# Optimization experiments

Hardware: AMD Instinct MI355X
Metric: run time of the kernel (lower is better)

The kernel has to match this reference:

```python
import jax, jax.numpy as jnp
import numpy as np

B, T, H, W, DIN = 8, 16, 32, 32, 384
DOUT = 384
K = 2  # kernel_size == stride == downsample_ratio


def setup_inputs() -> dict:
    key = jax.random.key(0)
    ks = jax.random.split(key, 12)
    s_in = 1.0 / np.sqrt(DIN)
    s_out = 1.0 / np.sqrt(DOUT)
    s_hid = 1.0 / np.sqrt(2 * DOUT)
    return {
        "x": jax.random.normal(ks[0], (B, T, H, W, DIN), dtype=jnp.float32),
        "Wq": jax.random.normal(ks[1], (DIN, DOUT), dtype=jnp.float32) * s_in,
        "bq": jnp.zeros((DOUT,), jnp.float32),
        "Wk": jax.random.normal(ks[2], (DIN, DOUT), dtype=jnp.float32) * s_in,
        "bk": jnp.zeros((DOUT,), jnp.float32),
        "Wv": jax.random.normal(ks[3], (DIN, DOUT), dtype=jnp.float32) * s_in,
        "bv": jnp.zeros((DOUT,), jnp.float32),
        "W1": jax.random.normal(ks[4], (DOUT, 2 * DOUT), dtype=jnp.float32) * s_out,
        "b1": jnp.zeros((2 * DOUT,), jnp.float32),
        "W2": jax.random.normal(ks[5], (2 * DOUT, DOUT), dtype=jnp.float32) * s_hid,
        "b2": jnp.zeros((DOUT,), jnp.float32),
        "gamma": jnp.ones((DOUT,), jnp.float32),
        "beta": jnp.zeros((DOUT,), jnp.float32),
    }


def _forward(x, Wq, bq, Wk, bk, Wv, bv, W1, b1, W2, b2, gamma, beta):
    b, t, h, w, d = x.shape
    nh, nw = h // K, w // K
    # window partition: (b*t, nh*nw, K*K, d)
    xw = x.reshape(b * t, nh, K, nw, K, d).transpose(0, 1, 3, 2, 4, 5)
    xw = xw.reshape(b * t, nh * nw, K * K, d)
    # mean-query local attention
    q = xw.mean(axis=2, keepdims=True) @ Wq + bq          # (bt, N, 1, D)
    k = xw @ Wk + bk                                       # (bt, N, K*K, D)
    v = xw @ Wv + bv                                       # (bt, N, K*K, D)
    scale = DOUT ** (-0.5)
    attn = jnp.einsum('bnqd,bnkd->bnqk', q, k) * scale     # (bt, N, 1, K*K)
    attn = jax.nn.softmax(attn, axis=-1)
    out = jnp.einsum('bnqk,bnkd->bnqd', attn, v)[:, :, 0]  # (bt, N, D)
    out = out.reshape(b, t, nh, nw, DOUT)
    # refine: Linear-GELU-Linear-LayerNorm (exact erf GELU, eps=1e-5)
    hdn = jax.nn.gelu(out @ W1 + b1, approximate=False)
    y = hdn @ W2 + b2
    mu = y.mean(axis=-1, keepdims=True)
    var = y.var(axis=-1, keepdims=True)
    y = (y - mu) * jax.lax.rsqrt(var + 1e-5) * gamma + beta
    return y


def reference(x, Wq, bq, Wk, bk, Wv, bv, W1, b1, W2, b2, gamma, beta):
    return _forward(x, Wq, bq, Wk, bk, Wv, bv, W1, b1, W2, b2, gamma, beta)
```

## Files before the change

### kernel.cpp

```cpp
#include <hip/hip_runtime.h>
#include <hip/hip_bf16.h>
#include <math.h>

typedef unsigned short u16;
typedef __attribute__((ext_vector_type(8))) short short8;
typedef __attribute__((ext_vector_type(4))) float f32x4;
typedef __attribute__((ext_vector_type(4))) unsigned short u16x4;

#define NWIN 32768
#define ROWSTRIDE (32*384)

__device__ __forceinline__ float b2f(u16 v) {
  unsigned int u = ((unsigned int)v) << 16;
  return __builtin_bit_cast(float, u);
}
__device__ __forceinline__ u16 f2b(float f) {
  unsigned int u = __builtin_bit_cast(unsigned int, f);
  unsigned int r = (u + 0x7fffu + ((u >> 16) & 1u)) >> 16;
  return (u16)r;
}

__global__ void fold_qk(const float* __restrict__ Wq, const float* __restrict__ Wk,
                        u16* __restrict__ WqkT) {
  __shared__ float a[16][17];
  __shared__ float b[16][17];
  const int tx = threadIdx.x, ty = threadIdx.y;
  const int k0 = blockIdx.x * 16, n0 = blockIdx.y * 16;
  float acc = 0.f;
  for (int d0 = 0; d0 < 384; d0 += 16) {
    a[ty][tx] = Wk[(n0 + ty) * 384 + d0 + tx];
    b[ty][tx] = Wq[(k0 + ty) * 384 + d0 + tx];
    __syncthreads();
#pragma unroll
    for (int dd = 0; dd < 16; ++dd) acc += a[ty][dd] * b[tx][dd];
    __syncthreads();
  }
  WqkT[(n0 + ty) * 384 + k0 + tx] = f2b(acc);
}

__global__ void bias_qk(const float* __restrict__ bq, const float* __restrict__ Wk,
                        float* __restrict__ bqk) {
  const int n = blockIdx.x * 128 + threadIdx.x;
  float s = 0.f;
  for (int d = 0; d < 384; ++d) s += bq[d] * Wk[n * 384 + d];
  bqk[n] = s;
}

__global__ void fold_v1(const float* __restrict__ Wv, const float* __restrict__ W1,
                        u16* __restrict__ W1pT) {
  __shared__ float a[16][17];
  __shared__ float b[16][17];
  const int tx = threadIdx.x, ty = threadIdx.y;
  const int n0 = blockIdx.x * 16, k0 = blockIdx.y * 16;
  float acc = 0.f;
  for (int d0 = 0; d0 < 384; d0 += 16) {
    a[ty][tx] = W1[(d0 + ty) * 768 + n0 + tx];
    b[ty][tx] = Wv[(k0 + ty) * 384 + d0 + tx];
    __syncthreads();
#pragma unroll
    for (int dd = 0; dd < 16; ++dd) acc += b[tx][dd] * a[dd][ty];
    __syncthreads();
  }
  W1pT[(n0 + ty) * 384 + k0 + tx] = f2b(acc);
}

__global__ void bias_v1(const float* __restrict__ bv, const float* __restrict__ W1,
                        const float* __restrict__ b1, float* __restrict__ b1p) {
  const int n = blockIdx.x * 256 + threadIdx.x;
  float s = b1[n];
  for (int d = 0; d < 384; ++d) s += bv[d] * W1[d * 768 + n];
  b1p[n] = s;
}

__global__ void tw2(const float* __restrict__ W2, u16* __restrict__ W2T) {
  const int g = blockIdx.x * 256 + threadIdx.x;
  const int n = g / 768, k = g - n * 768;
  W2T[g] = f2b(W2[k * 384 + n]);
}

__global__ void mean_kernel(const float* __restrict__ x, u16* __restrict__ xm) {
  const int g = blockIdx.x * 256 + threadIdx.x;
  const int w = g / 96;
  const int dv = g - w * 96;
  const int bt = w >> 8;
  const int ij = w & 255;
  const int i = ij >> 4, j = ij & 15;
  const float* xb = x + (size_t)((bt * 32 + 2 * i) * 32 + 2 * j) * 384 + dv * 4;
  const float4 a = *(const float4*)(xb);
  const float4 b = *(const float4*)(xb + 384);
  const float4 c = *(const float4*)(xb + ROWSTRIDE);
  const float4 d = *(const float4*)(xb + ROWSTRIDE + 384);
  u16x4 o;
  o.x = f2b(0.25f * (a.x + b.x + c.x + d.x));
  o.y = f2b(0.25f * (a.y + b.y + c.y + d.y));
  o.z = f2b(0.25f * (a.z + b.z + c.z + d.z));
  o.w = f2b(0.25f * (a.w + b.w + c.w + d.w));
  *(u16x4*)(xm + (size_t)w * 384 + dv * 4) = o;
}

template <int EPI>
__global__ __launch_bounds__(256) void gemm_bt(const u16* __restrict__ A,
                                               const u16* __restrict__ BT,
                                               const float* __restrict__ bias,
                                               u16* __restrict__ C, int N, int K) {
  __shared__ __align__(16) u16 As[128 * 64];
  __shared__ __align__(16) u16 Bs[128 * 64];
  const int tid = threadIdx.x;
  const int lane = tid & 63;
  const int wid = tid >> 6;
  const int wr = wid >> 1, wc = wid & 1;
  const int bm = blockIdx.x * 128;
  const int bn = blockIdx.y * 128;
  const int l15 = lane & 15;
  const int l4 = lane >> 4;

  f32x4 acc[4][4] = {};

  for (int kt = 0; kt < K; kt += 64) {
#pragma unroll
    for (int i = 0; i < 4; ++i) {
      const int c = i * 256 + tid;
      const int row = c >> 3, c8 = c & 7;
      const u16* ga = A + (size_t)(bm + row) * K + kt + c8 * 8;
      __builtin_amdgcn_global_load_lds((const __attribute__((address_space(1))) void*)ga,
                                       (__attribute__((address_space(3))) void*)&As[c * 8],
                                       16, 0, 0);
    }
#pragma unroll
    for (int i = 0; i < 4; ++i) {
      const int c = i * 256 + tid;
      const int row = c >> 3, c8 = c & 7;
      const u16* gb = BT + (size_t)(bn + row) * K + kt + c8 * 8;
      __builtin_amdgcn_global_load_lds((const __attribute__((address_space(1))) void*)gb,
                                       (__attribute__((address_space(3))) void*)&Bs[c * 8],
                                       16, 0, 0);
    }
    __syncthreads();
#pragma unroll
    for (int kk = 0; kk < 2; ++kk) {
      short8 af[4], bf[4];
#pragma unroll
      for (int mi = 0; mi < 4; ++mi)
        af[mi] = *(const short8*)&As[(wr * 64 + mi * 16 + l15) * 64 + kk * 32 + l4 * 8];
#pragma unroll
      for (int ni = 0; ni < 4; ++ni)
        bf[ni] = *(const short8*)&Bs[(wc * 64 + ni * 16 + l15) * 64 + kk * 32 + l4 * 8];
#pragma unroll
      for (int mi = 0; mi < 4; ++mi)
#pragma unroll
        for (int ni = 0; ni < 4; ++ni)
          acc[mi][ni] = __builtin_amdgcn_mfma_f32_16x16x32_bf16(af[mi], bf[ni], acc[mi][ni], 0, 0, 0);
    }
    __syncthreads();
  }

#pragma unroll
  for (int mi = 0; mi < 4; ++mi) {
#pragma unroll
    for (int ni = 0; ni < 4; ++ni) {
      const int col = bn + wc * 64 + ni * 16 + l15;
      const float bs = bias[col];
#pragma unroll
      for (int r = 0; r < 4; ++r) {
        const int row = bm + wr * 64 + mi * 16 + l4 * 4 + r;
        float v = acc[mi][ni][r] + bs;
        if (EPI == 1) v = 0.5f * v * (1.0f + erff(v * 0.70710678118654752f));
        C[(size_t)row * N + col] = f2b(v);
      }
    }
  }
}

__global__ void attn_kernel(const float* __restrict__ x, const u16* __restrict__ U,
                            u16* __restrict__ Aout) {
  const int tid = threadIdx.x;
  const int lane = tid & 63;
  const int w = blockIdx.x * 4 + (tid >> 6);
  const int bt = w >> 8;
  const int ij = w & 255;
  const int i = ij >> 4, j = ij & 15;
  const float* xb = x + (size_t)((bt * 32 + 2 * i) * 32 + 2 * j) * 384;
  float xv0[6], xv1[6], xv2[6], xv3[6];
  float d0 = 0.f, d1 = 0.f, d2 = 0.f, d3 = 0.f;
#pragma unroll
  for (int r = 0; r < 6; ++r) {
    const int d = r * 64 + lane;
    const float u = b2f(U[(size_t)w * 384 + d]);
    const float a = xb[d];
    const float b = xb[384 + d];
    const float c = xb[ROWSTRIDE + d];
    const float e = xb[ROWSTRIDE + 384 + d];
    xv0[r] = a; xv1[r] = b; xv2[r] = c; xv3[r] = e;
    d0 += a * u; d1 += b * u; d2 += c * u; d3 += e * u;
  }
#pragma unroll
  for (int off = 32; off > 0; off >>= 1) {
    d0 += __shfl_xor(d0, off, 64);
    d1 += __shfl_xor(d1, off, 64);
    d2 += __shfl_xor(d2, off, 64);
    d3 += __shfl_xor(d3, off, 64);
  }
  const float scale = 0.05103103630798287f;
  const float l0 = d0 * scale, l1 = d1 * scale, l2 = d2 * scale, l3 = d3 * scale;
  const float m = fmaxf(fmaxf(l0, l1), fmaxf(l2, l3));
  const float e0 = __expf(l0 - m), e1 = __expf(l1 - m), e2 = __expf(l2 - m), e3 = __expf(l3 - m);
  const float inv = 1.0f / (e0 + e1 + e2 + e3);
#pragma unroll
  for (int r = 0; r < 6; ++r) {
    const float a = (e0 * xv0[r] + e1 * xv1[r] + e2 * xv2[r] + e3 * xv3[r]) * inv;
    Aout[(size_t)w * 384 + r * 64 + lane] = f2b(a);
  }
}

__global__ void ln_kernel(const u16* __restrict__ Y, const float* __restrict__ gamma,
                          const float* __restrict__ beta, float* __restrict__ out) {
  const int tid = threadIdx.x;
  const int lane = tid & 63;
  const int w = blockIdx.x * 4 + (tid >> 6);
  float v[6];
  float s1 = 0.f, s2 = 0.f;
#pragma unroll
  for (int r = 0; r < 6; ++r) {
    v[r] = b2f(Y[(size_t)w * 384 + r * 64 + lane]);
    s1 += v[r];
    s2 += v[r] * v[r];
  }
#pragma unroll
  for (int off = 32; off > 0; off >>= 1) {
    s1 += __shfl_xor(s1, off, 64);
    s2 += __shfl_xor(s2, off, 64);
  }
  const float mu = s1 * (1.0f / 384.0f);
  const float var = s2 * (1.0f / 384.0f) - mu * mu;
  const float rstd = rsqrtf(var + 1e-5f);
#pragma unroll
  for (int r = 0; r < 6; ++r) {
    const int d = r * 64 + lane;
    out[(size_t)w * 384 + d] = (v[r] - mu) * rstd * gamma[d] + beta[d];
  }
}

extern "C" void kernel_launch(void* const* d_in, const int* in_sizes, int n_in,
                              void* d_out, int out_size, void* d_ws, size_t ws_size,
                              hipStream_t stream) {
  const float* x     = (const float*)d_in[0];
  const float* Wq    = (const float*)d_in[1];
  const float* bq    = (const float*)d_in[2];
  const float* Wk    = (const float*)d_in[3];
  const float* Wv    = (const float*)d_in[5];
  const float* bv    = (const float*)d_in[6];
  const float* W1    = (const float*)d_in[7];
  const float* b1    = (const float*)d_in[8];
  const float* W2    = (const float*)d_in[9];
  const float* b2    = (const float*)d_in[10];
  const float* gamma = (const float*)d_in[11];
  const float* beta  = (const float*)d_in[12];

  char* ws = (char*)d_ws;
  u16* Xmean = (u16*)(ws + 0);
  u16* Abuf  = Xmean;
  u16* Ubuf  = (u16*)(ws + 25165824);
  u16* Ypre  = Ubuf;
  u16* Hbuf  = (u16*)(ws + 50331648);
  char* wb   = ws + 100663296;
  u16*  WqkT = (u16*)(wb);
  u16*  W1pT = (u16*)(wb + 294912);
  u16*  W2T  = (u16*)(wb + 884736);
  float* bqk = (float*)(wb + 1474560);
  float* b1p = (float*)(wb + 1476096);

  fold_qk<<<dim3(24, 24), dim3(16, 16), 0, stream>>>(Wq, Wk, WqkT);
  bias_qk<<<3, 128, 0, stream>>>(bq, Wk, bqk);
  fold_v1<<<dim3(48, 24), dim3(16, 16), 0, stream>>>(Wv, W1, W1pT);
  bias_v1<<<3, 256, 0, stream>>>(bv, W1, b1, b1p);
  tw2<<<1152, 256, 0, stream>>>(W2, W2T);

  mean_kernel<<<12288, 256, 0, stream>>>(x, Xmean);
  gemm_bt<0><<<dim3(256, 3), 256, 0, stream>>>(Xmean, WqkT, bqk, Ubuf, 384, 384);
  attn_kernel<<<8192, 256, 0, stream>>>(x, Ubuf, Abuf);
  gemm_bt<1><<<dim3(256, 6), 256, 0, stream>>>(Abuf, W1pT, b1p, Hbuf, 768, 384);
  gemm_bt<0><<<dim3(256, 3), 256, 0, stream>>>(Hbuf, W2T, b2, Ypre, 384, 768);
  ln_kernel<<<8192, 256, 0, stream>>>(Ypre, gamma, beta, (float*)d_out);
}
```

Before: 562.3 us.

## Fuse pipeline into prologue, mean+QK GEMM+attention, and fused MLP+LayerNorm kernels

Replaces eleven launches with three. The five weight-folding kernels merge into one prologue. Window mean, the folded QK GEMM and the softmax attention now share one kernel, with U kept in shared memory. Both MLP GEMMs, GELU and LayerNorm run in one kernel that keeps the hidden activations in LDS. This removes the global round trips for Xmean, U, H and Ypre plus most launch overhead. The cost is lower grid parallelism: only 256 and 512 blocks with heavy LDS use, and the weight tiles are reloaded by every block.

```diff
diff --git a/kernel.cpp b/kernel.cpp
--- a/kernel.cpp
+++ b/kernel.cpp
@@ -20,117 +20,118 @@
   return (u16)r;
 }
 
-__global__ void fold_qk(const float* __restrict__ Wq, const float* __restrict__ Wk,
-                        u16* __restrict__ WqkT) {
-  __shared__ float a[16][17];
-  __shared__ float b[16][17];
-  const int tx = threadIdx.x, ty = threadIdx.y;
-  const int k0 = blockIdx.x * 16, n0 = blockIdx.y * 16;
-  float acc = 0.f;
-  for (int d0 = 0; d0 < 384; d0 += 16) {
-    a[ty][tx] = Wk[(n0 + ty) * 384 + d0 + tx];
-    b[ty][tx] = Wq[(k0 + ty) * 384 + d0 + tx];
-    __syncthreads();
-#pragma unroll
-    for (int dd = 0; dd < 16; ++dd) acc += a[ty][dd] * b[tx][dd];
-    __syncthreads();
-  }
-  WqkT[(n0 + ty) * 384 + k0 + tx] = f2b(acc);
-}
-
-__global__ void bias_qk(const float* __restrict__ bq, const float* __restrict__ Wk,
-                        float* __restrict__ bqk) {
-  const int n = blockIdx.x * 128 + threadIdx.x;
-  float s = 0.f;
-  for (int d = 0; d < 384; ++d) s += bq[d] * Wk[n * 384 + d];
-  bqk[n] = s;
-}
-
-__global__ void fold_v1(const float* __restrict__ Wv, const float* __restrict__ W1,
-                        u16* __restrict__ W1pT) {
-  __shared__ float a[16][17];
-  __shared__ float b[16][17];
-  const int tx = threadIdx.x, ty = threadIdx.y;
-  const int n0 = blockIdx.x * 16, k0 = blockIdx.y * 16;
-  float acc = 0.f;
-  for (int d0 = 0; d0 < 384; d0 += 16) {
-    a[ty][tx] = W1[(d0 + ty) * 768 + n0 + tx];
-    b[ty][tx] = Wv[(k0 + ty) * 384 + d0 + tx];
-    __syncthreads();
-#pragma unroll
-    for (int dd = 0; dd < 16; ++dd) acc += b[tx][dd] * a[dd][ty];
-    __syncthreads();
-  }
-  W1pT[(n0 + ty) * 384 + k0 + tx] = f2b(acc);
-}
-
-__global__ void bias_v1(const float* __restrict__ bv, const float* __restrict__ W1,
-                        const float* __restrict__ b1, float* __restrict__ b1p) {
-  const int n = blockIdx.x * 256 + threadIdx.x;
-  float s = b1[n];
-  for (int d = 0; d < 384; ++d) s += bv[d] * W1[d * 768 + n];
-  b1p[n] = s;
-}
-
-__global__ void tw2(const float* __restrict__ W2, u16* __restrict__ W2T) {
-  const int g = blockIdx.x * 256 + threadIdx.x;
-  const int n = g / 768, k = g - n * 768;
-  W2T[g] = f2b(W2[k * 384 + n]);
-}
-
-__global__ void mean_kernel(const float* __restrict__ x, u16* __restrict__ xm) {
-  const int g = blockIdx.x * 256 + threadIdx.x;
-  const int w = g / 96;
-  const int dv = g - w * 96;
-  const int bt = w >> 8;
-  const int ij = w & 255;
-  const int i = ij >> 4, j = ij & 15;
-  const float* xb = x + (size_t)((bt * 32 + 2 * i) * 32 + 2 * j) * 384 + dv * 4;
-  const float4 a = *(const float4*)(xb);
-  const float4 b = *(const float4*)(xb + 384);
-  const float4 c = *(const float4*)(xb + ROWSTRIDE);
-  const float4 d = *(const float4*)(xb + ROWSTRIDE + 384);
-  u16x4 o;
-  o.x = f2b(0.25f * (a.x + b.x + c.x + d.x));
-  o.y = f2b(0.25f * (a.y + b.y + c.y + d.y));
-  o.z = f2b(0.25f * (a.z + b.z + c.z + d.z));
-  o.w = f2b(0.25f * (a.w + b.w + c.w + d.w));
-  *(u16x4*)(xm + (size_t)w * 384 + dv * 4) = o;
-}
-
-template <int EPI>
-__global__ __launch_bounds__(256) void gemm_bt(const u16* __restrict__ A,
-                                               const u16* __restrict__ BT,
-                                               const float* __restrict__ bias,
-                                               u16* __restrict__ C, int N, int K) {
-  __shared__ __align__(16) u16 As[128 * 64];
-  __shared__ __align__(16) u16 Bs[128 * 64];
+__global__ __launch_bounds__(256) void prologue(
+    const float* __restrict__ Wq, const float* __restrict__ bq,
+    const float* __restrict__ Wk, const float* __restrict__ Wv,
+    const float* __restrict__ bv, const float* __restrict__ W1,
+    const float* __restrict__ b1, const float* __restrict__ W2,
+    u16* __restrict__ WqkT, u16* __restrict__ W1pT, u16* __restrict__ W2T,
+    float* __restrict__ bqk, float* __restrict__ b1p) {
+  __shared__ float sa[16][17];
+  __shared__ float sb[16][17];
+  const int b = blockIdx.x, t = threadIdx.x;
+  const int tx = t & 15, ty = t >> 4;
+  if (b < 576) {
+    const int k0 = (b % 24) * 16, n0 = (b / 24) * 16;
+    float acc = 0.f;
+    for (int d0 = 0; d0 < 384; d0 += 16) {
+      sa[ty][tx] = Wk[(n0 + ty) * 384 + d0 + tx];
+      sb[ty][tx] = Wq[(k0 + ty) * 384 + d0 + tx];
+      __syncthreads();
+#pragma unroll
+      for (int dd = 0; dd < 16; ++dd) acc += sa[ty][dd] * sb[tx][dd];
+      __syncthreads();
+    }
+    WqkT[(n0 + ty) * 384 + k0 + tx] = f2b(acc);
+  } else if (b < 1728) {
+    const int bb = b - 576;
+    const int n0 = (bb % 48) * 16, k0 = (bb / 48) * 16;
+    float acc = 0.f;
+    for (int d0 = 0; d0 < 384; d0 += 16) {
+      sa[ty][tx] = W1[(d0 + ty) * 768 + n0 + tx];
+      sb[ty][tx] = Wv[(k0 + ty) * 384 + d0 + tx];
+      __syncthreads();
+#pragma unroll
+      for (int dd = 0; dd < 16; ++dd) acc += sb[tx][dd] * sa[dd][ty];
+      __syncthreads();
+    }
+    W1pT[(n0 + ty) * 384 + k0 + tx] = f2b(acc);
+  } else if (b < 2880) {
+    const int g = (b - 1728) * 256 + t;
+    const int n = g / 768, k = g - n * 768;
+    W2T[g] = f2b(W2[k * 384 + n]);
+  } else if (b < 2976) {
+    const int lane = t & 63;
+    const int n = (b - 2880) * 4 + (t >> 6);
+    float s = 0.f;
+#pragma unroll
+    for (int rr = 0; rr < 6; ++rr) {
+      const int d = rr * 64 + lane;
+      s += bq[d] * Wk[n * 384 + d];
+    }
+#pragma unroll
+    for (int off = 32; off > 0; off >>= 1) s += __shfl_xor(s, off, 64);
+    if (lane == 0) bqk[n] = s;
+  } else {
+    const int lane = t & 63;
+    const int n = (b - 2976) * 4 + (t >> 6);
+    float s = 0.f;
+#pragma unroll
+    for (int rr = 0; rr < 6; ++rr) {
+      const int d = rr * 64 + lane;
+      s += bv[d] * W1[(size_t)d * 768 + n];
+    }
+#pragma unroll
+    for (int off = 32; off > 0; off >>= 1) s += __shfl_xor(s, off, 64);
+    if (lane == 0) b1p[n] = s + b1[n];
+  }
+}
+
+#define AS_STRIDE 72
+__global__ __launch_bounds__(512) void k2a(const float* __restrict__ x,
+                                           const u16* __restrict__ WqkT,
+                                           const float* __restrict__ bqk,
+                                           u16* __restrict__ Abuf) {
+  __shared__ __align__(16) u16 smem[128 * AS_STRIDE + 384 * 64];
+  u16* As = smem;
+  u16* Bs = smem + 128 * AS_STRIDE;
+  u16* Ubuf = smem;
+
   const int tid = threadIdx.x;
   const int lane = tid & 63;
   const int wid = tid >> 6;
-  const int wr = wid >> 1, wc = wid & 1;
-  const int bm = blockIdx.x * 128;
-  const int bn = blockIdx.y * 128;
+  const int wr = wid >> 2, wc = wid & 3;
   const int l15 = lane & 15;
   const int l4 = lane >> 4;
-
-  f32x4 acc[4][4] = {};
-
-  for (int kt = 0; kt < K; kt += 64) {
-#pragma unroll
-    for (int i = 0; i < 4; ++i) {
-      const int c = i * 256 + tid;
+  const int bm = blockIdx.x * 128;
+
+  f32x4 acc[4][6] = {};
+
+  for (int k0 = 0; k0 < 384; k0 += 64) {
+#pragma unroll
+    for (int s = 0; s < 4; ++s) {
+      const int c = s * 512 + tid;
+      const int row = c >> 4, d4 = c & 15;
+      const int w = bm + row;
+      const int bt = w >> 8, ij = w & 255;
+      const int wi = ij >> 4, wj = ij & 15;
+      const float* xb = x + (size_t)((bt * 32 + 2 * wi) * 32 + 2 * wj) * 384 + k0 + d4 * 4;
+      const float4 p0 = *(const float4*)(xb);
+      const float4 p1 = *(const float4*)(xb + 384);
+      const float4 p2 = *(const float4*)(xb + ROWSTRIDE);
+      const float4 p3 = *(const float4*)(xb + ROWSTRIDE + 384);
+      u16x4 o;
+      o.x = f2b(0.25f * (p0.x + p1.x + p2.x + p3.x));
+      o.y = f2b(0.25f * (p0.y + p1.y + p2.y + p3.y));
+      o.z = f2b(0.25f * (p0.z + p1.z + p2.z + p3.z));
+      o.w = f2b(0.25f * (p0.w + p1.w + p2.w + p3.w));
+      *(u16x4*)&As[row * AS_STRIDE + d4 * 4] = o;
+    }
+#pragma unroll
+    for (int s = 0; s < 6; ++s) {
+      const int c = s * 512 + tid;
       const int row = c >> 3, c8 = c & 7;
-      const u16* ga = A + (size_t)(bm + row) * K + kt + c8 * 8;
-      __builtin_amdgcn_global_load_lds((const __attribute__((address_space(1))) void*)ga,
-                                       (__attribute__((address_space(3))) void*)&As[c * 8],
-                                       16, 0, 0);
-    }
-#pragma unroll
-    for (int i = 0; i < 4; ++i) {
-      const int c = i * 256 + tid;
-      const int row = c >> 3, c8 = c & 7;
-      const u16* gb = BT + (size_t)(bn + row) * K + kt + c8 * 8;
+      const u16* gb = WqkT + (size_t)row * 384 + k0 + c8 * 8;
       __builtin_amdgcn_global_load_lds((const __attribute__((address_space(1))) void*)gb,
                                        (__attribute__((address_space(3))) void*)&Bs[c * 8],
                                        16, 0, 0);
@@ -138,106 +139,247 @@
     __syncthreads();
 #pragma unroll
     for (int kk = 0; kk < 2; ++kk) {
-      short8 af[4], bf[4];
-#pragma unroll
-      for (int mi = 0; mi < 4; ++mi)
-        af[mi] = *(const short8*)&As[(wr * 64 + mi * 16 + l15) * 64 + kk * 32 + l4 * 8];
-#pragma unroll
-      for (int ni = 0; ni < 4; ++ni)
-        bf[ni] = *(const short8*)&Bs[(wc * 64 + ni * 16 + l15) * 64 + kk * 32 + l4 * 8];
-#pragma unroll
-      for (int mi = 0; mi < 4; ++mi)
-#pragma unroll
-        for (int ni = 0; ni < 4; ++ni)
+      short8 af[4], bf[6];
+#pragma unroll
+      for (int mi = 0; mi < 4; ++mi)
+        af[mi] = *(const short8*)&As[(wr * 64 + mi * 16 + l15) * AS_STRIDE + kk * 32 + l4 * 8];
+#pragma unroll
+      for (int ni = 0; ni < 6; ++ni)
+        bf[ni] = *(const short8*)&Bs[(wc * 96 + ni * 16 + l15) * 64 + kk * 32 + l4 * 8];
+#pragma unroll
+      for (int mi = 0; mi < 4; ++mi)
+#pragma unroll
+        for (int ni = 0; ni < 6; ++ni)
           acc[mi][ni] = __builtin_amdgcn_mfma_f32_16x16x32_bf16(af[mi], bf[ni], acc[mi][ni], 0, 0, 0);
     }
     __syncthreads();
   }
 
-#pragma unroll
-  for (int mi = 0; mi < 4; ++mi) {
-#pragma unroll
-    for (int ni = 0; ni < 4; ++ni) {
-      const int col = bn + wc * 64 + ni * 16 + l15;
-      const float bs = bias[col];
-#pragma unroll
-      for (int r = 0; r < 4; ++r) {
-        const int row = bm + wr * 64 + mi * 16 + l4 * 4 + r;
-        float v = acc[mi][ni][r] + bs;
-        if (EPI == 1) v = 0.5f * v * (1.0f + erff(v * 0.70710678118654752f));
-        C[(size_t)row * N + col] = f2b(v);
-      }
-    }
-  }
-}
-
-__global__ void attn_kernel(const float* __restrict__ x, const u16* __restrict__ U,
-                            u16* __restrict__ Aout) {
+  const float scale = 0.05103103630798287f;
+#pragma unroll
+  for (int h = 0; h < 2; ++h) {
+    if (wr == h) {
+#pragma unroll
+      for (int mi = 0; mi < 4; ++mi)
+#pragma unroll
+        for (int ni = 0; ni < 6; ++ni) {
+          const int col = wc * 96 + ni * 16 + l15;
+          const float bk_ = bqk[col];
+#pragma unroll
+          for (int r = 0; r < 4; ++r) {
+            const int lr = mi * 16 + l4 * 4 + r;
+            Ubuf[lr * 388 + col] = f2b(acc[mi][ni][r] + bk_);
+          }
+        }
+    }
+    __syncthreads();
+#pragma unroll
+    for (int q = 0; q < 8; ++q) {
+      const int lr = wid * 8 + q;
+      const int w = bm + h * 64 + lr;
+      const int bt = w >> 8, ij = w & 255;
+      const int wi = ij >> 4, wj = ij & 15;
+      const float* xb = x + (size_t)((bt * 32 + 2 * wi) * 32 + 2 * wj) * 384;
+      float xv0[6], xv1[6], xv2[6], xv3[6];
+      float d0 = 0.f, d1 = 0.f, d2 = 0.f, d3 = 0.f;
+#pragma unroll
+      for (int rr = 0; rr < 6; ++rr) {
+        const int d = rr * 64 + lane;
+        const float u = b2f(Ubuf[lr * 388 + d]);
+        const float a = xb[d];
+        const float b = xb[384 + d];
+        const float c = xb[ROWSTRIDE + d];
+        const float e = xb[ROWSTRIDE + 384 + d];
+        xv0[rr] = a; xv1[rr] = b; xv2[rr] = c; xv3[rr] = e;
+        d0 += a * u; d1 += b * u; d2 += c * u; d3 += e * u;
+      }
+#pragma unroll
+      for (int off = 32; off > 0; off >>= 1) {
+        d0 += __shfl_xor(d0, off, 64);
+        d1 += __shfl_xor(d1, off, 64);
+        d2 += __shfl_xor(d2, off, 64);
+        d3 += __shfl_xor(d3, off, 64);
+      }
+      const float l0 = d0 * scale, l1 = d1 * scale, l2 = d2 * scale, l3 = d3 * scale;
+      const float m = fmaxf(fmaxf(l0, l1), fmaxf(l2, l3));
+      const float e0 = __expf(l0 - m), e1 = __expf(l1 - m), e2 = __expf(l2 - m), e3 = __expf(l3 - m);
+      const float inv = 1.0f / (e0 + e1 + e2 + e3);
+#pragma unroll
+      for (int rr = 0; rr < 6; ++rr) {
+        const float a = (e0 * xv0[rr] + e1 * xv1[rr] + e2 * xv2[rr] + e3 * xv3[rr]) * inv;
+        Abuf[(size_t)w * 384 + rr * 64 + lane] = f2b(a);
+      }
+    }
+    __syncthreads();
+  }
+}
+
+#define H_STRIDE 776
+__global__ __launch_bounds__(512) void mlp(const u16* __restrict__ Abuf,
+                                           const u16* __restrict__ W1pT,
+                                           const float* __restrict__ b1p,
+                                           const u16* __restrict__ W2T,
+                                           const float* __restrict__ b2,
+                                           const float* __restrict__ gamma,
+                                           const float* __restrict__ beta,
+                                           float* __restrict__ out) {
+  __shared__ __align__(16) u16 smem[77824];
+  u16* B1 = smem;
+  u16* A1 = smem + 49152;
+  u16* B2 = smem + 53248;
+  u16* H  = smem;
+  float* P1 = (float*)&smem[53248];
+  float* P2 = P1 + 512;
+  float* MU = P1 + 1024;
+  float* RS = P1 + 1088;
+
   const int tid = threadIdx.x;
   const int lane = tid & 63;
-  const int w = blockIdx.x * 4 + (tid >> 6);
-  const int bt = w >> 8;
-  const int ij = w & 255;
-  const int i = ij >> 4, j = ij & 15;
-  const float* xb = x + (size_t)((bt * 32 + 2 * i) * 32 + 2 * j) * 384;
-  float xv0[6], xv1[6], xv2[6], xv3[6];
-  float d0 = 0.f, d1 = 0.f, d2 = 0.f, d3 = 0.f;
-#pragma unroll
-  for (int r = 0; r < 6; ++r) {
-    const int d = r * 64 + lane;
-    const float u = b2f(U[(size_t)w * 384 + d]);
-    const float a = xb[d];
-    const float b = xb[384 + d];
-    const float c = xb[ROWSTRIDE + d];
-    const float e = xb[ROWSTRIDE + 384 + d];
-    xv0[r] = a; xv1[r] = b; xv2[r] = c; xv3[r] = e;
-    d0 += a * u; d1 += b * u; d2 += c * u; d3 += e * u;
-  }
-#pragma unroll
-  for (int off = 32; off > 0; off >>= 1) {
-    d0 += __shfl_xor(d0, off, 64);
-    d1 += __shfl_xor(d1, off, 64);
-    d2 += __shfl_xor(d2, off, 64);
-    d3 += __shfl_xor(d3, off, 64);
-  }
-  const float scale = 0.05103103630798287f;
-  const float l0 = d0 * scale, l1 = d1 * scale, l2 = d2 * scale, l3 = d3 * scale;
-  const float m = fmaxf(fmaxf(l0, l1), fmaxf(l2, l3));
-  const float e0 = __expf(l0 - m), e1 = __expf(l1 - m), e2 = __expf(l2 - m), e3 = __expf(l3 - m);
-  const float inv = 1.0f / (e0 + e1 + e2 + e3);
-#pragma unroll
-  for (int r = 0; r < 6; ++r) {
-    const float a = (e0 * xv0[r] + e1 * xv1[r] + e2 * xv2[r] + e3 * xv3[r]) * inv;
-    Aout[(size_t)w * 384 + r * 64 + lane] = f2b(a);
-  }
-}
-
-__global__ void ln_kernel(const u16* __restrict__ Y, const float* __restrict__ gamma,
-                          const float* __restrict__ beta, float* __restrict__ out) {
-  const int tid = threadIdx.x;
-  const int lane = tid & 63;
-  const int w = blockIdx.x * 4 + (tid >> 6);
-  float v[6];
-  float s1 = 0.f, s2 = 0.f;
-#pragma unroll
-  for (int r = 0; r < 6; ++r) {
-    v[r] = b2f(Y[(size_t)w * 384 + r * 64 + lane]);
-    s1 += v[r];
-    s2 += v[r] * v[r];
-  }
-#pragma unroll
-  for (int off = 32; off > 0; off >>= 1) {
-    s1 += __shfl_xor(s1, off, 64);
-    s2 += __shfl_xor(s2, off, 64);
-  }
-  const float mu = s1 * (1.0f / 384.0f);
-  const float var = s2 * (1.0f / 384.0f) - mu * mu;
-  const float rstd = rsqrtf(var + 1e-5f);
-#pragma unroll
-  for (int r = 0; r < 6; ++r) {
-    const int d = r * 64 + lane;
-    out[(size_t)w * 384 + d] = (v[r] - mu) * rstd * gamma[d] + beta[d];
-  }
+  const int wc = tid >> 6;
+  const int l15 = lane & 15;
+  const int l4 = lane >> 4;
+  const int w0 = blockIdx.x * 64;
+
+  f32x4 acc1[4][6] = {};
+  for (int k0 = 0; k0 < 384; k0 += 64) {
+    {
+      const int row = tid >> 3, c8 = tid & 7;
+      const u16* ga = Abuf + (size_t)(w0 + row) * 384 + k0 + c8 * 8;
+      __builtin_amdgcn_global_load_lds((const __attribute__((address_space(1))) void*)ga,
+                                       (__attribute__((address_space(3))) void*)&A1[tid * 8],
+                                       16, 0, 0);
+    }
+#pragma unroll
+    for (int s = 0; s < 12; ++s) {
+      const int c = s * 512 + tid;
+      const int row = c >> 3, c8 = c & 7;
+      const u16* gb = W1pT + (size_t)row * 384 + k0 + c8 * 8;
+      __builtin_amdgcn_global_load_lds((const __attribute__((address_space(1))) void*)gb,
+                                       (__attribute__((address_space(3))) void*)&B1[c * 8],
+                                       16, 0, 0);
+    }
+    __syncthreads();
+#pragma unroll
+    for (int kk = 0; kk < 2; ++kk) {
+      short8 af[4], bf[6];
+#pragma unroll
+      for (int mi = 0; mi < 4; ++mi)
+        af[mi] = *(const short8*)&A1[(mi * 16 + l15) * 64 + kk * 32 + l4 * 8];
+#pragma unroll
+      for (int ni = 0; ni < 6; ++ni)
+        bf[ni] = *(const short8*)&B1[(wc * 96 + ni * 16 + l15) * 64 + kk * 32 + l4 * 8];
+#pragma unroll
+      for (int mi = 0; mi < 4; ++mi)
+#pragma unroll
+        for (int ni = 0; ni < 6; ++ni)
+          acc1[mi][ni] = __builtin_amdgcn_mfma_f32_16x16x32_bf16(af[mi], bf[ni], acc1[mi][ni], 0, 0, 0);
+    }
+    __syncthreads();
+  }
+#pragma unroll
+  for (int mi = 0; mi < 4; ++mi)
+#pragma unroll
+    for (int ni = 0; ni < 6; ++ni) {
+      const int col = wc * 96 + ni * 16 + l15;
+      const float bc = b1p[col];
+#pragma unroll
+      for (int r = 0; r < 4; ++r) {
+        float v = acc1[mi][ni][r] + bc;
+        v = 0.5f * v * (1.0f + erff(v * 0.70710678118654752f));
+        H[(mi * 16 + l4 * 4 + r) * H_STRIDE + col] = f2b(v);
+      }
+    }
+  __syncthreads();
+
+  f32x4 acc2[4][3] = {};
+  for (int k0 = 0; k0 < 768; k0 += 64) {
+#pragma unroll
+    for (int s = 0; s < 6; ++s) {
+      const int c = s * 512 + tid;
+      const int row = c >> 3, c8 = c & 7;
+      const u16* gb = W2T + (size_t)row * 768 + k0 + c8 * 8;
+      __builtin_amdgcn_global_load_lds((const __attribute__((address_space(1))) void*)gb,
+                                       (__attribute__((address_space(3))) void*)&B2[c * 8],
+                                       16, 0, 0);
+    }
+    __syncthreads();
+#pragma unroll
+    for (int kk = 0; kk < 2; ++kk) {
+      short8 af[4], bf[3];
+#pragma unroll
+      for (int mi = 0; mi < 4; ++mi)
+        af[mi] = *(const short8*)&H[(mi * 16 + l15) * H_STRIDE + k0 + kk * 32 + l4 * 8];
+#pragma unroll
+      for (int ni = 0; ni < 3; ++ni)
+        bf[ni] = *(const short8*)&B2[(wc * 48 + ni * 16 + l15) * 64 + kk * 32 + l4 * 8];
+#pragma unroll
+      for (int mi = 0; mi < 4; ++mi)
+#pragma unroll
+        for (int ni = 0; ni < 3; ++ni)
+          acc2[mi][ni] = __builtin_amdgcn_mfma_f32_16x16x32_bf16(af[mi], bf[ni], acc2[mi][ni], 0, 0, 0);
+    }
+    __syncthreads();
+  }
+
+  float rs1[4][4], rs2[4][4];
+#pragma unroll
+  for (int mi = 0; mi < 4; ++mi)
+#pragma unroll
+    for (int r = 0; r < 4; ++r) {
+      float s1 = 0.f, s2 = 0.f;
+#pragma unroll
+      for (int ni = 0; ni < 3; ++ni) {
+        const int col = wc * 48 + ni * 16 + l15;
+        acc2[mi][ni][r] += b2[col];
+        const float v = acc2[mi][ni][r];
+        s1 += v; s2 += v * v;
+      }
+      rs1[mi][r] = s1; rs2[mi][r] = s2;
+    }
+#pragma unroll
+  for (int off = 1; off < 16; off <<= 1) {
+#pragma unroll
+    for (int mi = 0; mi < 4; ++mi)
+#pragma unroll
+      for (int r = 0; r < 4; ++r) {
+        rs1[mi][r] += __shfl_xor(rs1[mi][r], off, 64);
+        rs2[mi][r] += __shfl_xor(rs2[mi][r], off, 64);
+      }
+  }
+  if (l15 == 0) {
+#pragma unroll
+    for (int mi = 0; mi < 4; ++mi)
+#pragma unroll
+      for (int r = 0; r < 4; ++r) {
+        const int row = mi * 16 + l4 * 4 + r;
+        P1[row * 8 + wc] = rs1[mi][r];
+        P2[row * 8 + wc] = rs2[mi][r];
+      }
+  }
+  __syncthreads();
+  if (tid < 64) {
+    float s1 = 0.f, s2 = 0.f;
+#pragma unroll
+    for (int i = 0; i < 8; ++i) { s1 += P1[tid * 8 + i]; s2 += P2[tid * 8 + i]; }
+    const float mu = s1 * (1.0f / 384.0f);
+    const float var = s2 * (1.0f / 384.0f) - mu * mu;
+    MU[tid] = mu;
+    RS[tid] = rsqrtf(var + 1e-5f);
+  }
+  __syncthreads();
+#pragma unroll
+  for (int mi = 0; mi < 4; ++mi)
+#pragma unroll
+    for (int r = 0; r < 4; ++r) {
+      const int row = mi * 16 + l4 * 4 + r;
+      const float mu = MU[row], rstd = RS[row];
+#pragma unroll
+      for (int ni = 0; ni < 3; ++ni) {
+        const int col = wc * 48 + ni * 16 + l15;
+        out[(size_t)(w0 + row) * 384 + col] =
+            (acc2[mi][ni][r] - mu) * rstd * gamma[col] + beta[col];
+      }
+    }
 }
 
 extern "C" void kernel_launch(void* const* d_in, const int* in_sizes, int n_in,
@@ -257,28 +399,16 @@
   const float* beta  = (const float*)d_in[12];
 
   char* ws = (char*)d_ws;
-  u16* Xmean = (u16*)(ws + 0);
-  u16* Abuf  = Xmean;
-  u16* Ubuf  = (u16*)(ws + 25165824);
-  u16* Ypre  = Ubuf;
-  u16* Hbuf  = (u16*)(ws + 50331648);
-  char* wb   = ws + 100663296;
+  u16*  Abuf = (u16*)(ws + 0);
+  char* wb   = ws + 33554432;
   u16*  WqkT = (u16*)(wb);
   u16*  W1pT = (u16*)(wb + 294912);
   u16*  W2T  = (u16*)(wb + 884736);
   float* bqk = (float*)(wb + 1474560);
   float* b1p = (float*)(wb + 1476096);
 
-  fold_qk<<<dim3(24, 24), dim3(16, 16), 0, stream>>>(Wq, Wk, WqkT);
-  bias_qk<<<3, 128, 0, stream>>>(bq, Wk, bqk);
-  fold_v1<<<dim3(48, 24), dim3(16, 16), 0, stream>>>(Wv, W1, W1pT);
-  bias_v1<<<3, 256, 0, stream>>>(bv, W1, b1, b1p);
-  tw2<<<1152, 256, 0, stream>>>(W2, W2T);
-
-  mean_kernel<<<12288, 256, 0, stream>>>(x, Xmean);
-  gemm_bt<0><<<dim3(256, 3), 256, 0, stream>>>(Xmean, WqkT, bqk, Ubuf, 384, 384);
-  attn_kernel<<<8192, 256, 0, stream>>>(x, Ubuf, Abuf);
-  gemm_bt<1><<<dim3(256, 6), 256, 0, stream>>>(Abuf, W1pT, b1p, Hbuf, 768, 384);
-  gemm_bt<0><<<dim3(256, 3), 256, 0, stream>>>(Hbuf, W2T, b2, Ypre, 384, 768);
-  ln_kernel<<<8192, 256, 0, stream>>>(Ypre, gamma, beta, (float*)d_out);
-}
+  prologue<<<3168, 256, 0, stream>>>(Wq, bq, Wk, Wv, bv, W1, b1, W2,
+                                     WqkT, W1pT, W2T, bqk, b1p);
+  k2a<<<256, 512, 0, stream>>>(x, WqkT, bqk, Abuf);
+  mlp<<<512, 512, 0, stream>>>(Abuf, W1pT, b1p, W2T, b2, gamma, beta, (float*)d_out);
+}
```

Result: faster. 479.9 us (-14.7%).
